# Performance work log

Measured on AMD Instinct MI355X. Metric: run time of the kernel, lower is better.

Reference implementation:

```python
import jax, jax.numpy as jnp
import numpy as np

EPS = 1e-8


def decode_fcos_obb(loc, deltas):
    """FCOS-style OBB decode. deltas = (d_x-, d_y-, d_z-, d_x+, d_y+, d_z+, theta):
    distances from the point to the 6 box faces, measured in the box's yaw-rotated
    frame. Returns OBB (x, y, z, w, l, h, theta)."""
    theta = deltas[:, 6]
    w = deltas[:, 0] + deltas[:, 3]
    l = deltas[:, 1] + deltas[:, 4]
    h = deltas[:, 2] + deltas[:, 5]
    ox = (deltas[:, 3] - deltas[:, 0]) * 0.5
    oy = (deltas[:, 4] - deltas[:, 1]) * 0.5
    oz = (deltas[:, 5] - deltas[:, 2]) * 0.5
    c, s = jnp.cos(theta), jnp.sin(theta)
    cx = loc[:, 0] + ox * c - oy * s
    cy = loc[:, 1] + ox * s + oy * c
    cz = loc[:, 2] + oz
    return jnp.stack([cx, cy, cz, w, l, h, theta], axis=-1)


def box2corners(box):
    # box: (B,N,5) = (x,y,w,h,alpha) -> (B,N,4,2) CCW corners
    x, y, w, h, a = (box[..., i] for i in range(5))
    x4 = jnp.asarray([0.5, -0.5, -0.5, 0.5], box.dtype) * w[..., None]
    y4 = jnp.asarray([0.5, 0.5, -0.5, -0.5], box.dtype) * h[..., None]
    c, s = jnp.cos(a)[..., None], jnp.sin(a)[..., None]
    return jnp.stack([x4 * c - y4 * s + x[..., None],
                      x4 * s + y4 * c + y[..., None]], axis=-1)


def box_intersection(corners1, corners2):
    # Pairwise intersections of the 4 edges of box1 with the 4 edges of box2.
    # Returns points (B,N,4,4,2) and validity mask (B,N,4,4).
    l1 = jnp.concatenate([corners1, jnp.roll(corners1, -1, axis=2)], axis=-1)[:, :, :, None, :]
    l2 = jnp.concatenate([corners2, jnp.roll(corners2, -1, axis=2)], axis=-1)[:, :, None, :, :]
    x1, y1, x2, y2 = l1[..., 0], l1[..., 1], l1[..., 2], l1[..., 3]
    x3, y3, x4, y4 = l2[..., 0], l2[..., 1], l2[..., 2], l2[..., 3]
    num = (y4 - y3) * (x2 - x1) - (x4 - x3) * (y2 - y1)
    den_t = (x4 - x3) * (y1 - y3) - (y4 - y3) * (x1 - x3)
    den_u = (x2 - x1) * (y1 - y3) - (y2 - y1) * (x1 - x3)
    safe = jnp.where(num == 0., 1., num)
    t = jnp.where(num == 0., -1., den_t / safe)
    u = jnp.where(num == 0., -1., -den_u / safe)
    mask = (t > 0.) & (t < 1.) & (u > 0.) & (u < 1.)
    t2 = den_t / (num + EPS)
    pts = jnp.stack([x1 + t2 * (x2 - x1), y1 + t2 * (y2 - y1)], axis=-1)
    pts = pts * mask[..., None].astype(pts.dtype)
    return pts, mask


def box1_in_box2(corners1, corners2):
    # Which corners of box1 lie inside box2 (projection onto box2's edge frame).
    a = corners2[:, :, 0:1, :]
    b = corners2[:, :, 1:2, :]
    d = corners2[:, :, 3:4, :]
    ab, ad, am = b - a, d - a, corners1 - a
    p_ab = (ab * am).sum(-1) / (ab * ab).sum(-1)
    p_ad = (ad * am).sum(-1) / (ad * ad).sum(-1)
    tol = 1e-6
    return (p_ab > -tol) & (p_ab < 1 + tol) & (p_ad > -tol) & (p_ad < 1 + tol)


def sorted_polygon_area(vertices, mask):
    # vertices: (B,N,24,2) candidate polygon vertices, mask: (B,N,24) validity.
    # Sort valid vertices CCW around their centroid, pad with the first vertex,
    # shoelace area. Equivalent to Rotated_IoU's sort_vertices + calculate_area.
    m = mask.astype(vertices.dtype)
    nv = m.sum(-1)  # (B,N) number of valid vertices
    mean = (vertices * m[..., None]).sum(2) / jnp.maximum(nv, 1.)[..., None]
    v = vertices - mean[:, :, None, :]
    ang = jnp.where(mask, jnp.arctan2(v[..., 1], v[..., 0]), 1e6)  # invalid -> last
    idx = jnp.argsort(ang, axis=-1)
    vs = jnp.take_along_axis(v, idx[..., None], axis=2)
    pos = jnp.arange(vertices.shape[2])
    pad = pos[None, None, :] >= nv[..., None]
    vs = jnp.where(pad[..., None], vs[:, :, :1, :], vs)  # pad with first valid vertex
    nxt = jnp.roll(vs, -1, axis=2)
    cross = vs[..., 0] * nxt[..., 1] - vs[..., 1] * nxt[..., 0]
    return 0.5 * jnp.abs(cross.sum(-1))


def cal_iou(box1, box2):
    c1 = box2corners(box1)
    c2 = box2corners(box2)
    pts, m_i = box_intersection(c1, c2)
    B, N = box1.shape[:2]
    vertices = jnp.concatenate([c1, c2, pts.reshape(B, N, 16, 2)], axis=2)
    mask = jnp.concatenate([box1_in_box2(c1, c2), box1_in_box2(c2, c1),
                            m_i.reshape(B, N, 16)], axis=2)
    inter = sorted_polygon_area(vertices, mask)
    u = box1[..., 2] * box1[..., 3] + box2[..., 2] * box2[..., 3] - inter
    return inter / u, u


def cal_iou_3d(b1, b2):
    # boxes: (B,N,7) = (x,y,z,w,l,h,theta); 2D rotated IoU in xy, overlap in z.
    box1 = jnp.stack([b1[..., 0], b1[..., 1], b1[..., 3], b1[..., 4], b1[..., 6]], -1)
    box2 = jnp.stack([b2[..., 0], b2[..., 1], b2[..., 3], b2[..., 4], b2[..., 6]], -1)
    zmax1, zmin1 = b1[..., 2] + b1[..., 5] * 0.5, b1[..., 2] - b1[..., 5] * 0.5
    zmax2, zmin2 = b2[..., 2] + b2[..., 5] * 0.5, b2[..., 2] - b2[..., 5] * 0.5
    z_overlap = jnp.clip(jnp.minimum(zmax1, zmax2) - jnp.maximum(zmin1, zmin2), 0.)
    iou_2d, u = cal_iou(box1, box2)
    inter_3d = iou_2d * u * z_overlap
    v1 = b1[..., 3] * b1[..., 4] * b1[..., 5]
    v2 = b2[..., 3] * b2[..., 4] * b2[..., 5]
    u3d = v1 + v2 - inter_3d
    return inter_3d / u3d, u3d


def rotated_iou_loss(pred, target, weight):
    loc = jnp.zeros((pred.shape[0], 3), pred.dtype)
    pb = decode_fcos_obb(loc, pred)[None]     # (1,N,7)
    tb = decode_fcos_obb(loc, target)[None]   # (1,N,7)
    ious, unions = cal_iou_3d(pb, tb)
    vol_inter = ious * unions
    ious = (vol_inter + 1.0) / (unions + 1.0)  # smoothed IoU
    losses = -jnp.log(ious)
    return (losses * weight).sum()


def setup_inputs():
    key = jax.random.key(0)
    k1, k2, k3 = jax.random.split(key, 3)
    N = 250000

    def make_deltas(k):
        u = jax.random.uniform(k, (N, 7), dtype=jnp.float32)
        dists = u[:, :6] * 2.0 + 0.3               # positive face distances
        theta = (u[:, 6:7] - 0.5) * jnp.pi          # yaw in (-pi/2, pi/2)
        return jnp.concatenate([dists, theta], axis=1)

    return {
        "pred": make_deltas(k1),
        "target": make_deltas(k2),
        "weight": jax.random.uniform(k3, (N,), dtype=jnp.float32),
    }


def reference(pred, target, weight):
    return rotated_iou_loss(pred, target, weight)
```

## Files before the change

kernel.cpp:

```cpp
#include <hip/hip_runtime.h>
#include <math.h>


#define RCP(x) __builtin_amdgcn_rcpf(x)

__global__ __launch_bounds__(256, 2) void riou_loss_kernel(
    const float* __restrict__ pred, const float* __restrict__ tgt,
    const float* __restrict__ wgt, float* __restrict__ out, int n)
{
    int i = blockIdx.x * blockDim.x + threadIdx.x;
    float loss = 0.0f;
    if (i < n) {
        const float* pp = pred + 7 * i;
        const float* qq = tgt + 7 * i;
        float p0 = pp[0], p1 = pp[1], p2 = pp[2], p3 = pp[3], p4 = pp[4], p5 = pp[5], p6 = pp[6];
        float q0 = qq[0], q1 = qq[1], q2 = qq[2], q3 = qq[3], q4 = qq[4], q5 = qq[5], q6 = qq[6];

        float w1 = p0 + p3, l1 = p1 + p4, h1 = p2 + p5;
        float ox1 = (p3 - p0) * 0.5f, oy1 = (p4 - p1) * 0.5f, oz1 = (p5 - p2) * 0.5f;
        float sA = __sinf(p6), cA = __cosf(p6);
        float cx1 = ox1 * cA - oy1 * sA, cy1 = ox1 * sA + oy1 * cA;

        float w2 = q0 + q3, l2 = q1 + q4, h2 = q2 + q5;
        float ox2 = (q3 - q0) * 0.5f, oy2 = (q4 - q1) * 0.5f, oz2 = (q5 - q2) * 0.5f;
        float sB = __sinf(q6), cB = __cosf(q6);
        float cx2 = ox2 * cB - oy2 * sB, cy2 = ox2 * sB + oy2 * cB;

        float hw1 = 0.5f * w1, hl1 = 0.5f * l1;
        float c1x0 =  hw1 * cA - hl1 * sA + cx1, c1y0 =  hw1 * sA + hl1 * cA + cy1;
        float c1x1 = -hw1 * cA - hl1 * sA + cx1, c1y1 = -hw1 * sA + hl1 * cA + cy1;
        float c1x2 = -hw1 * cA + hl1 * sA + cx1, c1y2 = -hw1 * sA - hl1 * cA + cy1;
        float c1x3 =  hw1 * cA + hl1 * sA + cx1, c1y3 =  hw1 * sA - hl1 * cA + cy1;
        float hw2 = 0.5f * w2, hl2 = 0.5f * l2;
        float c2x0 =  hw2 * cB - hl2 * sB + cx2, c2y0 =  hw2 * sB + hl2 * cB + cy2;
        float c2x1 = -hw2 * cB - hl2 * sB + cx2, c2y1 = -hw2 * sB + hl2 * cB + cy2;
        float c2x2 = -hw2 * cB + hl2 * sB + cx2, c2y2 = -hw2 * sB - hl2 * cB + cy2;
        float c2x3 =  hw2 * cB + hl2 * sB + cx2, c2y3 =  hw2 * sB - hl2 * cB + cy2;

        float sumx = 0.0f, sumy = 0.0f;
        int nv = 0;
#define ACC(M, X, Y) { sumx += (M) ? (X) : 0.0f; sumy += (M) ? (Y) : 0.0f; nv += (M) ? 1 : 0; }

        const float TOL = 1e-6f;
        float abxB = c2x1 - c2x0, abyB = c2y1 - c2y0;
        float adxB = c2x3 - c2x0, adyB = c2y3 - c2y0;
        float rabB = RCP(abxB * abxB + abyB * abyB);
        float radB = RCP(adxB * adxB + adyB * adyB);
#define PIB_B(MX, MY, M) { float amx = (MX) - c2x0, amy = (MY) - c2y0; \
        float pab = (abxB * amx + abyB * amy) * rabB; \
        float pdd = (adxB * amx + adyB * amy) * radB; \
        M = (pab > -TOL) & (pab < 1.0f + TOL) & (pdd > -TOL) & (pdd < 1.0f + TOL); }
        bool mA0, mA1, mA2, mA3;
        PIB_B(c1x0, c1y0, mA0) PIB_B(c1x1, c1y1, mA1)
        PIB_B(c1x2, c1y2, mA2) PIB_B(c1x3, c1y3, mA3)
        ACC(mA0, c1x0, c1y0) ACC(mA1, c1x1, c1y1) ACC(mA2, c1x2, c1y2) ACC(mA3, c1x3, c1y3)
        float abxA = c1x1 - c1x0, abyA = c1y1 - c1y0;
        float adxA = c1x3 - c1x0, adyA = c1y3 - c1y0;
        float rabA = RCP(abxA * abxA + abyA * abyA);
        float radA = RCP(adxA * adxA + adyA * adyA);
#define PIB_A(MX, MY, M) { float amx = (MX) - c1x0, amy = (MY) - c1y0; \
        float pab = (abxA * amx + abyA * amy) * rabA; \
        float pdd = (adxA * amx + adyA * amy) * radA; \
        M = (pab > -TOL) & (pab < 1.0f + TOL) & (pdd > -TOL) & (pdd < 1.0f + TOL); }
        bool mB0, mB1, mB2, mB3;
        PIB_A(c2x0, c2y0, mB0) PIB_A(c2x1, c2y1, mB1)
        PIB_A(c2x2, c2y2, mB2) PIB_A(c2x3, c2y3, mB3)
        ACC(mB0, c2x0, c2y0) ACC(mB1, c2x1, c2y1) ACC(mB2, c2x2, c2y2) ACC(mB3, c2x3, c2y3)

#define ISECT(X1, Y1, X2, Y2, X3, Y3, X4, Y4, PX, PY, M) { \
        float ex = (X2) - (X1), ey = (Y2) - (Y1); \
        float fx = (X4) - (X3), fy = (Y4) - (Y3); \
        float gx = (X1) - (X3), gy = (Y1) - (Y3); \
        float num = fy * ex - fx * ey; \
        float dt_ = fx * gy - fy * gx; \
        float du_ = ex * gy - ey * gx; \
        float rr = RCP(num); \
        float tt = dt_ * rr, uu = -du_ * rr; \
        M = (tt > 0.0f) & (tt < 1.0f) & (uu > 0.0f) & (uu < 1.0f); \
        PX = (X1) + tt * ex; PY = (Y1) + tt * ey; }
#define SITEM(PX, PY, M, OX0, OY0, OX1, OY1, CNT) { \
        bool tk0 = (M) && ((CNT) == 0); bool tk1 = (M) && ((CNT) == 1); \
        OX0 = tk0 ? (PX) : OX0; OY0 = tk0 ? (PY) : OY0; \
        OX1 = tk1 ? (PX) : OX1; OY1 = tk1 ? (PY) : OY1; \
        CNT += (M) ? 1 : 0; }
#define EDGE_GROUP(X1, Y1, X2, Y2, EX0, EY0, EM0, EX1, EY1, EM1) { \
        int gc = 0; float px, py; bool mm; \
        ISECT(X1, Y1, X2, Y2, c2x0, c2y0, c2x1, c2y1, px, py, mm) \
        ACC(mm, px, py) SITEM(px, py, mm, EX0, EY0, EX1, EY1, gc) \
        ISECT(X1, Y1, X2, Y2, c2x1, c2y1, c2x2, c2y2, px, py, mm) \
        ACC(mm, px, py) SITEM(px, py, mm, EX0, EY0, EX1, EY1, gc) \
        ISECT(X1, Y1, X2, Y2, c2x2, c2y2, c2x3, c2y3, px, py, mm) \
        ACC(mm, px, py) SITEM(px, py, mm, EX0, EY0, EX1, EY1, gc) \
        ISECT(X1, Y1, X2, Y2, c2x3, c2y3, c2x0, c2y0, px, py, mm) \
        ACC(mm, px, py) SITEM(px, py, mm, EX0, EY0, EX1, EY1, gc) \
        EM0 = (gc > 0); EM1 = (gc > 1); }

        float vx8 = 0.f, vy8 = 0.f, vx9 = 0.f, vy9 = 0.f;   bool m8, m9;
        float vx10 = 0.f, vy10 = 0.f, vx11 = 0.f, vy11 = 0.f; bool m10, m11;
        float vx12 = 0.f, vy12 = 0.f, vx13 = 0.f, vy13 = 0.f; bool m12, m13;
        float vx14 = 0.f, vy14 = 0.f, vx15 = 0.f, vy15 = 0.f; bool m14, m15;
        EDGE_GROUP(c1x0, c1y0, c1x1, c1y1, vx8, vy8, m8, vx9, vy9, m9)
        EDGE_GROUP(c1x1, c1y1, c1x2, c1y2, vx10, vy10, m10, vx11, vy11, m11)
        EDGE_GROUP(c1x2, c1y2, c1x3, c1y3, vx12, vy12, m12, vx13, vy13, m13)
        EDGE_GROUP(c1x3, c1y3, c1x0, c1y0, vx14, vy14, m14, vx15, vy15, m15)

        float vx0 = c1x0, vy0 = c1y0, vx1 = c1x1, vy1 = c1y1;
        float vx2 = c1x2, vy2 = c1y2, vx3 = c1x3, vy3 = c1y3;
        float vx4 = c2x0, vy4 = c2y0, vx5 = c2x1, vy5 = c2y1;
        float vx6 = c2x2, vy6 = c2y2, vx7 = c2x3, vy7 = c2y3;
        bool m0 = mA0, m1 = mA1, m2 = mA2, m3 = mA3;
        bool m4 = mB0, m5 = mB1, m6 = mB2, m7 = mB3;

        float inv_nv = RCP(fmaxf((float)nv, 1.0f));
        float mx_ = sumx * inv_nv, my_ = sumy * inv_nv;
        float ang0, ang1, ang2, ang3, ang4, ang5, ang6, ang7;
        float ang8, ang9, ang10, ang11, ang12, ang13, ang14, ang15;
#define ANG(K) { vx##K -= mx_; vy##K -= my_; \
        float dd = vy##K * RCP(fmaxf(fabsf(vx##K) + fabsf(vy##K), 1e-38f)); \
        ang##K = m##K ? ((vx##K >= 0.0f) ? dd : copysignf(2.0f, vy##K) - dd) : 1e6f; }
        ANG(0) ANG(1) ANG(2) ANG(3) ANG(4) ANG(5) ANG(6) ANG(7)
        ANG(8) ANG(9) ANG(10) ANG(11) ANG(12) ANG(13) ANG(14) ANG(15)

#define CE(A, B) { bool sw = ang##A > ang##B; \
        float t0 = ang##A, t1 = ang##B; ang##A = sw ? t1 : t0; ang##B = sw ? t0 : t1; \
        float u0 = vx##A, u1 = vx##B;   vx##A = sw ? u1 : u0;  vx##B = sw ? u0 : u1; \
        float w0 = vy##A, w1 = vy##B;   vy##A = sw ? w1 : w0;  vy##B = sw ? w0 : w1; }
        CE(0,1) CE(2,3) CE(4,5) CE(6,7) CE(8,9) CE(10,11) CE(12,13) CE(14,15)
        CE(0,2) CE(1,3) CE(4,6) CE(5,7) CE(8,10) CE(9,11) CE(12,14) CE(13,15)
        CE(1,2) CE(5,6) CE(9,10) CE(13,14)
        CE(0,4) CE(1,5) CE(2,6) CE(3,7) CE(8,12) CE(9,13) CE(10,14) CE(11,15)
        CE(2,4) CE(3,5) CE(10,12) CE(11,13)
        CE(1,2) CE(3,4) CE(5,6) CE(9,10) CE(11,12) CE(13,14)
        CE(0,8) CE(1,9) CE(2,10) CE(3,11) CE(4,12) CE(5,13) CE(6,14) CE(7,15)
        CE(4,8) CE(5,9) CE(6,10) CE(7,11)
        CE(2,4) CE(3,5) CE(6,8) CE(7,9) CE(10,12) CE(11,13)
        CE(1,2) CE(3,4) CE(5,6) CE(7,8) CE(9,10) CE(11,12) CE(13,14)

#define PAD(K) { bool pd = ((K) >= nv); vx##K = pd ? vx0 : vx##K; vy##K = pd ? vy0 : vy##K; }
        PAD(1) PAD(2) PAD(3) PAD(4) PAD(5) PAD(6) PAD(7) PAD(8)
        PAD(9) PAD(10) PAD(11) PAD(12) PAD(13) PAD(14) PAD(15)

        float cs = 0.0f;
#define SHOE(A, B) cs += vx##A * vy##B - vy##A * vx##B;
        SHOE(0,1) SHOE(1,2) SHOE(2,3) SHOE(3,4) SHOE(4,5) SHOE(5,6) SHOE(6,7) SHOE(7,8)
        SHOE(8,9) SHOE(9,10) SHOE(10,11) SHOE(11,12) SHOE(12,13) SHOE(13,14) SHOE(14,15) SHOE(15,0)
        float inter = 0.5f * fabsf(cs);

        float zmax1 = oz1 + h1 * 0.5f, zmin1 = oz1 - h1 * 0.5f;
        float zmax2 = oz2 + h2 * 0.5f, zmin2 = oz2 - h2 * 0.5f;
        float zo = fmaxf(fminf(zmax1, zmax2) - fmaxf(zmin1, zmin2), 0.0f);
        float inter3d = inter * zo;
        float vol1 = w1 * l1 * h1, vol2 = w2 * l2 * h2;
        float u3d = vol1 + vol2 - inter3d;
        float iouf = (inter3d + 1.0f) * RCP(u3d + 1.0f);
        loss = -__logf(iouf) * wgt[i];
    }

#pragma unroll
    for (int off = 32; off > 0; off >>= 1)
        loss += __shfl_down(loss, off, 64);
    __shared__ float wsum[4];
    int lane = threadIdx.x & 63, wid = threadIdx.x >> 6;
    if (lane == 0) wsum[wid] = loss;
    __syncthreads();
    if (threadIdx.x == 0) {
        float s = wsum[0] + wsum[1] + wsum[2] + wsum[3];
        atomicAdd(out, s);
    }
}

extern "C" void kernel_launch(void* const* d_in, const int* in_sizes, int n_in,
                              void* d_out, int out_size, void* d_ws, size_t ws_size,
                              hipStream_t stream) {
    const float* pred = (const float*)d_in[0];
    const float* tgt  = (const float*)d_in[1];
    const float* wgt  = (const float*)d_in[2];
    float* out = (float*)d_out;
    int n = in_sizes[2];

    hipMemsetAsync(out, 0, sizeof(float), stream);
    int block = 256;
    int grid = (n + block - 1) / block;
    riou_loss_kernel<<<grid, block, 0, stream>>>(pred, tgt, wgt, out, n);
}
```

Measured before the change: 83.01 us.

## Pack sort payload to bf16 pairs, use single-wave blocks with per-wave atomics

Each vertex's centered x and y are packed into one 32-bit word (truncated to bf16 precision), so the 16-element sorting network moves one register per element instead of two, and the angle swap becomes min/max. Blocks shrink to one wavefront, which removes the shared-memory reduction and barrier but gives four times as many atomicAdds to the output. The z-overlap and volume math is hoisted ahead of the polygon work to shorten live ranges. Truncating coordinates to bf16 lowers the precision of the shoelace area, and padding now tests the angle sentinel instead of the vertex count.

```diff
diff --git a/kernel.cpp b/kernel.cpp
--- a/kernel.cpp
+++ b/kernel.cpp
@@ -4,11 +4,11 @@
 
 #define RCP(x) __builtin_amdgcn_rcpf(x)
 
-__global__ __launch_bounds__(256, 2) void riou_loss_kernel(
+__global__ __launch_bounds__(64, 4) void riou_loss_kernel(
     const float* __restrict__ pred, const float* __restrict__ tgt,
     const float* __restrict__ wgt, float* __restrict__ out, int n)
 {
-    int i = blockIdx.x * blockDim.x + threadIdx.x;
+    int i = blockIdx.x * 64 + threadIdx.x;
     float loss = 0.0f;
     if (i < n) {
         const float* pp = pred + 7 * i;
@@ -17,14 +17,20 @@
         float q0 = qq[0], q1 = qq[1], q2 = qq[2], q3 = qq[3], q4 = qq[4], q5 = qq[5], q6 = qq[6];
 
         float w1 = p0 + p3, l1 = p1 + p4, h1 = p2 + p5;
-        float ox1 = (p3 - p0) * 0.5f, oy1 = (p4 - p1) * 0.5f, oz1 = (p5 - p2) * 0.5f;
+        float oz1 = (p5 - p2) * 0.5f;
+        float ox1 = (p3 - p0) * 0.5f, oy1 = (p4 - p1) * 0.5f;
         float sA = __sinf(p6), cA = __cosf(p6);
         float cx1 = ox1 * cA - oy1 * sA, cy1 = ox1 * sA + oy1 * cA;
 
         float w2 = q0 + q3, l2 = q1 + q4, h2 = q2 + q5;
-        float ox2 = (q3 - q0) * 0.5f, oy2 = (q4 - q1) * 0.5f, oz2 = (q5 - q2) * 0.5f;
+        float oz2 = (q5 - q2) * 0.5f;
+        float ox2 = (q3 - q0) * 0.5f, oy2 = (q4 - q1) * 0.5f;
         float sB = __sinf(q6), cB = __cosf(q6);
         float cx2 = ox2 * cB - oy2 * sB, cy2 = ox2 * sB + oy2 * cB;
+
+        float vol1 = w1 * l1 * h1, vol2 = w2 * l2 * h2;
+        float zo = fmaxf(fminf(oz1 + h1 * 0.5f, oz2 + h2 * 0.5f) -
+                         fmaxf(oz1 - h1 * 0.5f, oz2 - h2 * 0.5f), 0.0f);
 
         float hw1 = 0.5f * w1, hl1 = 0.5f * l1;
         float c1x0 =  hw1 * cA - hl1 * sA + cx1, c1y0 =  hw1 * sA + hl1 * cA + cy1;
@@ -115,16 +121,21 @@
         float mx_ = sumx * inv_nv, my_ = sumy * inv_nv;
         float ang0, ang1, ang2, ang3, ang4, ang5, ang6, ang7;
         float ang8, ang9, ang10, ang11, ang12, ang13, ang14, ang15;
-#define ANG(K) { vx##K -= mx_; vy##K -= my_; \
-        float dd = vy##K * RCP(fmaxf(fabsf(vx##K) + fabsf(vy##K), 1e-38f)); \
-        ang##K = m##K ? ((vx##K >= 0.0f) ? dd : copysignf(2.0f, vy##K) - dd) : 1e6f; }
-        ANG(0) ANG(1) ANG(2) ANG(3) ANG(4) ANG(5) ANG(6) ANG(7)
-        ANG(8) ANG(9) ANG(10) ANG(11) ANG(12) ANG(13) ANG(14) ANG(15)
+        unsigned pk0, pk1, pk2, pk3, pk4, pk5, pk6, pk7;
+        unsigned pk8, pk9, pk10, pk11, pk12, pk13, pk14, pk15;
+#define ANGPACK(K) { float xc = vx##K - mx_, yc = vy##K - my_; \
+        float dd = yc * RCP(fmaxf(fabsf(xc) + fabsf(yc), 1e-38f)); \
+        ang##K = m##K ? ((xc >= 0.0f) ? dd : copysignf(2.0f, yc) - dd) : 1e6f; \
+        pk##K = (__float_as_uint(xc) & 0xFFFF0000u) | (__float_as_uint(yc) >> 16); }
+        ANGPACK(0) ANGPACK(1) ANGPACK(2) ANGPACK(3)
+        ANGPACK(4) ANGPACK(5) ANGPACK(6) ANGPACK(7)
+        ANGPACK(8) ANGPACK(9) ANGPACK(10) ANGPACK(11)
+        ANGPACK(12) ANGPACK(13) ANGPACK(14) ANGPACK(15)
 
 #define CE(A, B) { bool sw = ang##A > ang##B; \
-        float t0 = ang##A, t1 = ang##B; ang##A = sw ? t1 : t0; ang##B = sw ? t0 : t1; \
-        float u0 = vx##A, u1 = vx##B;   vx##A = sw ? u1 : u0;  vx##B = sw ? u0 : u1; \
-        float w0 = vy##A, w1 = vy##B;   vy##A = sw ? w1 : w0;  vy##B = sw ? w0 : w1; }
+        float mn = fminf(ang##A, ang##B), mx2 = fmaxf(ang##A, ang##B); \
+        ang##A = mn; ang##B = mx2; \
+        unsigned ta = pk##A; pk##A = sw ? pk##B : pk##A; pk##B = sw ? ta : pk##B; }
         CE(0,1) CE(2,3) CE(4,5) CE(6,7) CE(8,9) CE(10,11) CE(12,13) CE(14,15)
         CE(0,2) CE(1,3) CE(4,6) CE(5,7) CE(8,10) CE(9,11) CE(12,14) CE(13,15)
         CE(1,2) CE(5,6) CE(9,10) CE(13,14)
@@ -136,21 +147,21 @@
         CE(2,4) CE(3,5) CE(6,8) CE(7,9) CE(10,12) CE(11,13)
         CE(1,2) CE(3,4) CE(5,6) CE(7,8) CE(9,10) CE(11,12) CE(13,14)
 
-#define PAD(K) { bool pd = ((K) >= nv); vx##K = pd ? vx0 : vx##K; vy##K = pd ? vy0 : vy##K; }
+#define PAD(K) { pk##K = (ang##K > 5e5f) ? pk0 : pk##K; }
         PAD(1) PAD(2) PAD(3) PAD(4) PAD(5) PAD(6) PAD(7) PAD(8)
         PAD(9) PAD(10) PAD(11) PAD(12) PAD(13) PAD(14) PAD(15)
 
+#define UPX(K) float ux##K = __uint_as_float(pk##K & 0xFFFF0000u); \
+               float uy##K = __uint_as_float(pk##K << 16);
+        UPX(0) UPX(1) UPX(2) UPX(3) UPX(4) UPX(5) UPX(6) UPX(7)
+        UPX(8) UPX(9) UPX(10) UPX(11) UPX(12) UPX(13) UPX(14) UPX(15)
         float cs = 0.0f;
-#define SHOE(A, B) cs += vx##A * vy##B - vy##A * vx##B;
+#define SHOE(A, B) cs += ux##A * uy##B - uy##A * ux##B;
         SHOE(0,1) SHOE(1,2) SHOE(2,3) SHOE(3,4) SHOE(4,5) SHOE(5,6) SHOE(6,7) SHOE(7,8)
         SHOE(8,9) SHOE(9,10) SHOE(10,11) SHOE(11,12) SHOE(12,13) SHOE(13,14) SHOE(14,15) SHOE(15,0)
         float inter = 0.5f * fabsf(cs);
 
-        float zmax1 = oz1 + h1 * 0.5f, zmin1 = oz1 - h1 * 0.5f;
-        float zmax2 = oz2 + h2 * 0.5f, zmin2 = oz2 - h2 * 0.5f;
-        float zo = fmaxf(fminf(zmax1, zmax2) - fmaxf(zmin1, zmin2), 0.0f);
         float inter3d = inter * zo;
-        float vol1 = w1 * l1 * h1, vol2 = w2 * l2 * h2;
         float u3d = vol1 + vol2 - inter3d;
         float iouf = (inter3d + 1.0f) * RCP(u3d + 1.0f);
         loss = -__logf(iouf) * wgt[i];
@@ -159,14 +170,7 @@
 #pragma unroll
     for (int off = 32; off > 0; off >>= 1)
         loss += __shfl_down(loss, off, 64);
-    __shared__ float wsum[4];
-    int lane = threadIdx.x & 63, wid = threadIdx.x >> 6;
-    if (lane == 0) wsum[wid] = loss;
-    __syncthreads();
-    if (threadIdx.x == 0) {
-        float s = wsum[0] + wsum[1] + wsum[2] + wsum[3];
-        atomicAdd(out, s);
-    }
+    if (threadIdx.x == 0) atomicAdd(out, loss);
 }
 
 extern "C" void kernel_launch(void* const* d_in, const int* in_sizes, int n_in,
@@ -179,7 +183,7 @@
     int n = in_sizes[2];
 
     hipMemsetAsync(out, 0, sizeof(float), stream);
-    int block = 256;
+    int block = 64;
     int grid = (n + block - 1) / block;
     riou_loss_kernel<<<grid, block, 0, stream>>>(pred, tgt, wgt, out, n);
 }
```

Result: slower. 117.3 us (+41.3%).
